# Kernel tuning notes

Measured on AMD Instinct MI355X. Metric: run time of the kernel, lower is better.

Reference implementation:

```python
import jax, jax.numpy as jnp
import numpy as np

N_DIMS = 64
D1 = N_DIMS - 1          # 63, feature dim of xs and of per-head q/k/v in non-last layers
N_EMBD = 2 * N_DIMS      # 128, forced by H + attn residual
N_LAYER = 12
N_HEAD = 4
POINTS = 512
BS = 16
LN_EPS = 1e-5


def setup_inputs() -> dict:
    key = jax.random.key(0)
    ks = jax.random.split(key, 16)
    s = 0.05
    f32 = jnp.float32
    inp = {
        "xs": jax.random.normal(ks[0], (BS, POINTS, D1), f32),
        "ys": jax.random.normal(ks[1], (BS, POINTS), f32),
        "head_mask": jnp.ones((1, N_HEAD, 1, 1), f32),
        # _read_in
        "read_in_W": jax.random.normal(ks[2], (N_DIMS, N_EMBD), f32) * s,
        "read_in_b": jnp.zeros((N_EMBD,), f32),
        # layers 0..n_layer-2: q/v Linear(D1 -> n_head*D1), key linear is unused (identity repeat)
        "qW": jax.random.normal(ks[3], (N_LAYER - 1, D1, N_HEAD * D1), f32) * s,
        "vW": jax.random.normal(ks[4], (N_LAYER - 1, D1, N_HEAD * D1), f32) * s,
        # last layer: q/k/v Linear(n_embd -> n_head*n_embd)
        "qW_last": jax.random.normal(ks[5], (N_EMBD, N_HEAD * N_EMBD), f32) * s,
        "kW_last": jax.random.normal(ks[6], (N_EMBD, N_HEAD * N_EMBD), f32) * s,
        "vW_last": jax.random.normal(ks[7], (N_EMBD, N_HEAD * N_EMBD), f32) * s,
        # layernorms
        "ln1_g": jnp.ones((N_LAYER, N_EMBD), f32),
        "ln1_b": jnp.zeros((N_LAYER, N_EMBD), f32),
        "ln2_g": jnp.ones((N_LAYER, N_EMBD), f32),
        "ln2_b": jnp.zeros((N_LAYER, N_EMBD), f32),
        # MLPs (n_embd -> 4*n_embd -> n_embd)
        "mlp_W1": jax.random.normal(ks[8], (N_LAYER, N_EMBD, 4 * N_EMBD), f32) * s,
        "mlp_b1": jnp.zeros((N_LAYER, 4 * N_EMBD), f32),
        "mlp_W2": jax.random.normal(ks[9], (N_LAYER, 4 * N_EMBD, N_EMBD), f32) * s,
        "mlp_b2": jnp.zeros((N_LAYER, N_EMBD), f32),
        # _read_out
        "read_out_W": jax.random.normal(ks[10], (N_EMBD, 1), f32) * s,
        "read_out_b": jnp.zeros((1,), f32),
    }
    return inp


def _layernorm(x, g, b):
    mu = jnp.mean(x, axis=-1, keepdims=True)
    var = jnp.var(x, axis=-1, keepdims=True)
    return (x - mu) * jax.lax.rsqrt(var + LN_EPS) * g + b


def _forward(xs, ys, head_mask, read_in_W, read_in_b, qW, vW,
             qW_last, kW_last, vW_last, ln1_g, ln1_b, ln2_g, ln2_b,
             mlp_W1, mlp_b1, mlp_W2, mlp_b2, read_out_W, read_out_b):
    bs, P, d = xs.shape  # d = n_dims - 1
    # _combine: interleave x (zero-padded) and (x, y) rows -> [bs, 2P, n_dims]
    xs_e = jnp.concatenate([xs, jnp.zeros((bs, P, 1), xs.dtype)], axis=2)
    ys_w = jnp.concatenate([xs, ys[:, :, None]], axis=2)
    zs = jnp.stack([xs_e, ys_w], axis=2).reshape(bs, 2 * P, d + 1)
    N = 2 * P

    # triangular count-normalization: row i (0-based) has 1/(i+1) on cols <= i
    i = jnp.arange(N)
    maskNorm = jnp.where(i[None, :] <= i[:, None], 1.0 / (i[:, None] + 1.0), 0.0).astype(xs.dtype)

    H = zs @ read_in_W + read_in_b  # [bs, N, n_embd]

    for idx in range(N_LAYER):
        if idx != N_LAYER - 1:
            # q from the "label half" of H, k is identity on the "feature half", v learned
            q = (H[:, :, N_DIMS:2 * N_DIMS - 1] @ qW[idx]).reshape(bs, N, N_HEAD, D1).transpose(0, 2, 1, 3)
            k = jnp.broadcast_to(H[:, None, :, :D1], (bs, N_HEAD, N, D1))
            v = (H[:, :, :D1] @ vW[idx]).reshape(bs, N, N_HEAD, D1).transpose(0, 2, 1, 3)
            # cat((z1[n_dims zeros], ., z2[1 zero])) -> head dim 2*n_dims == n_embd
            pad = ((0, 0), (0, 0), (0, 0), (N_DIMS, 1))
            q = jnp.pad(q, pad) * head_mask
            k = jnp.pad(k, pad) * head_mask
            v = jnp.pad(v, pad) * head_mask
        else:
            q = (H @ qW_last).reshape(bs, N, N_HEAD, N_EMBD).transpose(0, 2, 1, 3) * head_mask
            k = (H @ kW_last).reshape(bs, N, N_HEAD, N_EMBD).transpose(0, 2, 1, 3) * head_mask
            v = (H @ vW_last).reshape(bs, N, N_HEAD, N_EMBD).transpose(0, 2, 1, 3) * head_mask
        scores = jax.nn.relu(jnp.einsum('bhid,bhjd->bhij', q, k)) * maskNorm  # [bs,h,N,N]
        attn = jnp.einsum('bhij,bhjd->bhid', scores, v).sum(axis=1)           # [bs,N,n_embd]
        H = _layernorm(H + attn, ln1_g[idx], ln1_b[idx])
        mlp = jax.nn.relu(H @ mlp_W1[idx] + mlp_b1[idx]) @ mlp_W2[idx] + mlp_b2[idx]
        H = _layernorm(H + mlp, ln2_g[idx], ln2_b[idx])

    pred = H @ read_out_W + read_out_b  # [bs, N, 1]
    return pred[:, ::2, 0]              # [bs, P]


def reference(xs, ys, head_mask, read_in_W, read_in_b, qW, vW,
              qW_last, kW_last, vW_last, ln1_g, ln1_b, ln2_g, ln2_b,
              mlp_W1, mlp_b1, mlp_W2, mlp_b2, read_out_W, read_out_b):
    return _forward(xs, ys, head_mask, read_in_W, read_in_b, qW, vW,
                    qW_last, kW_last, vW_last, ln1_g, ln1_b, ln2_g, ln2_b,
                    mlp_W1, mlp_b1, mlp_W2, mlp_b2, read_out_W, read_out_b)
```

## Files before the change

### kernel.cpp

```cpp
#include <hip/hip_runtime.h>

#define BS 16
#define SEQ 1024
#define EMB 128
#define NHEAD 4
#define LN_EPS 1e-5f

typedef __attribute__((ext_vector_type(8))) short bf16x8;
typedef __attribute__((ext_vector_type(8))) _Float16 f16x8;
typedef __attribute__((ext_vector_type(4))) float f32x4;
typedef __attribute__((ext_vector_type(4))) unsigned short u16x4;
typedef __attribute__((ext_vector_type(4))) unsigned int u32x4;

__device__ __forceinline__ unsigned short f2b(float f) {
  union { float f; unsigned u; } v; v.f = f;
  unsigned r = v.u + 0x7fff + ((v.u >> 16) & 1);
  return (unsigned short)(r >> 16);
}
__device__ __forceinline__ float b2f(unsigned short u) {
  return __uint_as_float((unsigned)u << 16);
}
__device__ __forceinline__ unsigned short f2h(float f) {
  union { _Float16 h; unsigned short u; } v; v.h = (_Float16)f; return v.u;
}
__device__ __forceinline__ void split2(float x, unsigned short& hi, unsigned short& lo) {
  unsigned short h = f2b(x);
  float hf = __uint_as_float((unsigned)h << 16);
  hi = h; lo = f2b(x - hf);
}
__device__ __forceinline__ float rsqrt_acc(float v) {
  float r = rsqrtf(v);
  return r * (1.5f - 0.5f * v * r * r);
}

__global__ void k_prep_fragT(const float* __restrict__ in, unsigned short* __restrict__ out,
                             size_t PL, int L, int Kin, int Nin, int N, int K) {
  int idx = blockIdx.x * 256 + threadIdx.x;
  int nblk = (N >> 4) * (K >> 5);
  int total = L * N * K;
  if (idx >= total) return;
  int e = idx & 7;
  int lane = (idx >> 3) & 63;
  int blk = (idx >> 9) % nblk;
  int l = idx / (512 * nblk);
  int nb = blk % (N >> 4), kc = blk / (N >> 4);
  int n = nb * 16 + (lane & 15);
  int k = kc * 32 + (lane >> 4) * 8 + e;
  float v = (k < Kin && n < Nin) ? in[(size_t)l * Kin * Nin + (size_t)k * Nin + n] : 0.f;
  unsigned short hi, lo; split2(v, hi, lo);
  out[idx] = hi; out[PL + idx] = lo;
}

__global__ void k_prep_qvfrag(const float* __restrict__ qW, const float* __restrict__ vW,
                              unsigned short* __restrict__ out, size_t PL) {
  int idx = blockIdx.x * 256 + threadIdx.x;
  int total = 11 * 512 * 128;
  if (idx >= total) return;
  int e = idx & 7;
  int lane = (idx >> 3) & 63;
  int blk = (idx >> 9) & 127;
  int l = idx >> 16;
  int nb = blk & 31, kc = blk >> 5;
  int n = nb * 16 + (lane & 15);
  int k = kc * 32 + (lane >> 4) * 8 + e;
  float v = 0.f;
  if (n < 256) {
    int hh = n >> 6, d = n & 63;
    if (d < 63 && k >= 64 && k < 127) v = qW[(size_t)l * 63 * 252 + (size_t)(k - 64) * 252 + hh * 63 + d];
  } else {
    int n2 = n - 256, hh = n2 >> 6, d = n2 & 63;
    if (d < 63 && k < 63) v = vW[(size_t)l * 63 * 252 + (size_t)k * 252 + hh * 63 + d];
  }
  unsigned short hi, lo; split2(v, hi, lo);
  out[idx] = hi; out[PL + idx] = lo;
}

__global__ void k_prep_lastfrag(const float* __restrict__ qW, const float* __restrict__ kW,
                                const float* __restrict__ vW,
                                unsigned short* __restrict__ out, size_t PL) {
  int idx = blockIdx.x * 256 + threadIdx.x;
  int total = 1536 * 128;
  if (idx >= total) return;
  int e = idx & 7;
  int lane = (idx >> 3) & 63;
  int blk = idx >> 9;
  int nb = blk % 96, kc = blk / 96;
  int n = nb * 16 + (lane & 15);
  int k = kc * 32 + (lane >> 4) * 8 + e;
  int tsel = n >> 9, n2 = n & 511;
  const float* W = tsel == 0 ? qW : (tsel == 1 ? kW : vW);
  float v = W[(size_t)k * 512 + n2];
  unsigned short hi, lo; split2(v, hi, lo);
  out[idx] = hi; out[PL + idx] = lo;
}

__global__ void k_combine_readin(const float* __restrict__ xs, const float* __restrict__ ys,
                                 const float* __restrict__ W, const float* __restrict__ bias,
                                 unsigned short* __restrict__ Hbf, size_t hbPl,
                                 unsigned short* __restrict__ Hh) {
  int blk = blockIdx.x;
  int b = blk >> 10, t = blk & 1023, p = t >> 1;
  __shared__ float zs[64];
  int tid = threadIdx.x;
  if (tid < 64) {
    float v;
    if (tid < 63) v = xs[((size_t)b * 512 + p) * 63 + tid];
    else v = (t & 1) ? ys[(size_t)b * 512 + p] : 0.f;
    zs[tid] = v;
  }
  __syncthreads();
  float acc = bias[tid];
  #pragma unroll 8
  for (int d = 0; d < 64; ++d) acc += zs[d] * W[d * 128 + tid];
  size_t o = (size_t)blk * 128 + tid;
  unsigned short hi, lo; split2(acc, hi, lo);
  Hbf[o] = hi; Hbf[hbPl + o] = lo;
  if (tid < 64) Hh[(size_t)blk * 64 + tid] = f2h(acc);
}

template<int MODE, bool RELU>
__global__ __launch_bounds__(256) void k_gemm(
    const unsigned short* __restrict__ A, size_t aPl,
    const unsigned short* __restrict__ BT, size_t bPl, const float* __restrict__ bias,
    int N,
    unsigned short* __restrict__ out0,
    unsigned short* __restrict__ out1,
    unsigned short* __restrict__ out2) {
  extern __shared__ unsigned short lds[];
  int tid = threadIdx.x;
  int wid = tid >> 6, lane = tid & 63;
  int lr = lane & 15, lg = lane >> 4;
  int row0g = blockIdx.x * 64;
  int n0 = blockIdx.y * 64;
  unsigned short* Ah = lds;
  unsigned short* Al = Ah + 64 * 136;
  {
    const unsigned short* gA = A + (size_t)row0g * 128;
    const unsigned short* srcs[2] = { gA, gA + aPl };
    unsigned short* dsts[2] = { Ah, Al };
    #pragma unroll
    for (int p = 0; p < 2; ++p)
      #pragma unroll
      for (int it = 0; it < 4; ++it) {
        int e = it * 2048 + tid * 8;
        bf16x8 v = *reinterpret_cast<const bf16x8*>(srcs[p] + e);
        *reinterpret_cast<bf16x8*>(dsts[p] + (e >> 7) * 136 + (e & 127)) = v;
      }
  }
  __syncthreads();
  bf16x8 afh[4], afl[4];
  #pragma unroll
  for (int kf = 0; kf < 4; ++kf) {
    int o = (wid * 16 + lr) * 136 + kf * 32 + lg * 8;
    afh[kf] = *reinterpret_cast<const bf16x8*>(Ah + o);
    afl[kf] = *reinterpret_cast<const bf16x8*>(Al + o);
  }
  f32x4 acc[4] = {};
  int nhw = N >> 4;
  #pragma unroll
  for (int nf = 0; nf < 4; ++nf) {
    #pragma unroll
    for (int kf = 0; kf < 4; ++kf) {
      size_t bo = ((size_t)kf * nhw + (n0 >> 4) + nf) * 512 + lane * 8;
      bf16x8 bh = *reinterpret_cast<const bf16x8*>(BT + bo);
      bf16x8 bl = *reinterpret_cast<const bf16x8*>(BT + bPl + bo);
      acc[nf] = __builtin_amdgcn_mfma_f32_16x16x32_bf16(afh[kf], bh, acc[nf], 0, 0, 0);
      acc[nf] = __builtin_amdgcn_mfma_f32_16x16x32_bf16(afl[kf], bh, acc[nf], 0, 0, 0);
      acc[nf] = __builtin_amdgcn_mfma_f32_16x16x32_bf16(afh[kf], bl, acc[nf], 0, 0, 0);
    }
  }
  __syncthreads();
  #pragma unroll
  for (int nf = 0; nf < 4; ++nf) {
    int c = n0 + nf * 16 + lr;
    float bv = bias ? bias[c] : 0.f;
    #pragma unroll
    for (int r = 0; r < 4; ++r) {
      float v = acc[nf][r] + bv;
      if (RELU) v = fmaxf(v, 0.f);
      int rL = wid * 16 + lg * 4 + r, cL = nf * 16 + lr;
      ((unsigned short(*)[66])lds)[rL][cL] = f2h(v);
    }
  }
  __syncthreads();
  int u = tid * 2;
  int lane2 = u >> 3, e0 = u & 7;
  if (MODE == 2) {
    unsigned short (*t16)[66] = (unsigned short(*)[66])lds;
    int b = row0g >> 10, t0 = row0g & 1023;
    int tsel = n0 >> 9, c2b = n0 & 511, hh = c2b >> 7, dbase = c2b & 127;
    size_t bh = (size_t)b * NHEAD + hh;
    if (tsel < 2) {
      unsigned short* base = tsel ? out1 : out0;
      int tb0 = t0 >> 4, kc0 = dbase >> 5;
      #pragma unroll
      for (int fb = 0; fb < 8; ++fb) {
        int tbl = fb >> 1, kcl = fb & 1;
        int t_l = tbl * 16 + (lane2 & 15);
        int c_l = kcl * 32 + ((lane2 >> 4) << 3) + e0;
        size_t dst = ((bh * 64 + tb0 + tbl) * 4 + kc0 + kcl) * 512 + lane2 * 8 + e0;
        base[dst] = t16[t_l][c_l];
        base[dst + 1] = t16[t_l][c_l + 1];
      }
    } else {
      int db0 = dbase >> 4, jc0 = t0 >> 5;
      #pragma unroll
      for (int fb = 0; fb < 8; ++fb) {
        int dbl = fb >> 1, jcl = fb & 1;
        int c_l = dbl * 16 + (lane2 & 15);
        int t_l = jcl * 32 + ((lane2 >> 4) << 3) + e0;
        size_t dst = ((bh * 8 + db0 + dbl) * 32 + jc0 + jcl) * 512 + lane2 * 8 + e0;
        out2[dst] = t16[t_l][c_l];
        out2[dst + 1] = t16[t_l + 1][c_l];
      }
    }
  } else {
    unsigned short (*t16)[66] = (unsigned short(*)[66])lds;
    int b = row0g >> 10, t0 = row0g & 1023;
    if (n0 < 256) {
      size_t bh = (size_t)b * NHEAD + (n0 >> 6);
      int tb0 = t0 >> 4;
      #pragma unroll
      for (int fb = 0; fb < 8; ++fb) {
        int tbl = fb >> 1, kcl = fb & 1;
        int t_l = tbl * 16 + (lane2 & 15);
        int c_l = kcl * 32 + ((lane2 >> 4) << 3) + e0;
        size_t dst = ((bh * 64 + tb0 + tbl) * 2 + kcl) * 512 + lane2 * 8 + e0;
        out0[dst] = t16[t_l][c_l];
        out0[dst + 1] = t16[t_l][c_l + 1];
      }
    } else {
      size_t bh = (size_t)b * NHEAD + ((n0 - 256) >> 6);
      int jc0 = t0 >> 5;
      #pragma unroll
      for (int fb = 0; fb < 8; ++fb) {
        int dbl = fb >> 1, jcl = fb & 1;
        int c_l = dbl * 16 + (lane2 & 15);
        int t_l = jcl * 32 + ((lane2 >> 4) << 3) + e0;
        size_t dst = ((bh * 4 + dbl) * 32 + jc0 + jcl) * 512 + lane2 * 8 + e0;
        out1[dst] = t16[t_l][c_l];
        out1[dst + 1] = t16[t_l + 1][c_l];
      }
    }
  }
}

__global__ __launch_bounds__(512) void k_attn_v7(
    const unsigned short* __restrict__ q,
    const unsigned short* __restrict__ Hh,
    const unsigned short* __restrict__ vT,
    const float* __restrict__ head_mask,
    const unsigned short* __restrict__ HbfIn, unsigned short* __restrict__ HbfOut, size_t hbPl,
    const float* __restrict__ g, const float* __restrict__ bta) {
  extern __shared__ char sh[];
  int bid = blockIdx.x;
  int xcd = bid & 7, u = bid >> 3;
  int b = xcd * 2 + (u >> 4);
  int pidx = u & 15;
  int tid = threadIdx.x;
  int wid = tid >> 6, lane = tid & 63;
  int h = wid & 3, grp = wid >> 2;
  int lr = lane & 15, lg = lane >> 4;
  int i0t[2] = { pidx * 32, (31 - pidx) * 32 };
  int NSS = (33 - pidx) >> 1;

  const char* gK = (const char*)(Hh + (size_t)b * SEQ * 64);
  char* KB = sh;
  unsigned short* sw = (unsigned short*)(sh + 16384 + wid * 2560);

  const unsigned short* qh = q + (size_t)(b * NHEAD + h) * 65536;
  const unsigned short* vh = vT + (size_t)(b * NHEAD + h) * 65536;

  f16x8 qf[2][2][2];
  #pragma unroll
  for (int t = 0; t < 2; ++t)
    #pragma unroll
    for (int mf = 0; mf < 2; ++mf)
      #pragma unroll
      for (int kf = 0; kf < 2; ++kf)
        qf[t][mf][kf] = *reinterpret_cast<const f16x8*>(
            qh + ((((i0t[t] >> 4) + mf) * 2 + kf) << 9) + lane * 8);
  f32x4 oacc[2][2][4] = {};

  u32x4 sreg;
  auto SLOAD = [&](int ss) {
    sreg = *reinterpret_cast<const u32x4*>(gK + (size_t)ss * 8192 + tid * 16);
  };
  auto SWRITE = [&](int buf) {
    int row = tid >> 3, colb = (tid & 7) * 16;
    *reinterpret_cast<u32x4*>(KB + buf * 8192 + row * 128 + (colb ^ ((row & 7) << 4))) = sreg;
  };

  SLOAD(0); SWRITE(0);
  __syncthreads();

  for (int ss = 0; ss < NSS; ++ss) {
    int cur = ss & 1;
    bool more = (ss + 1 < NSS);
    if (more) SLOAD(ss + 1);
    int js = ss * 64 + grp * 32;
    if (js < i0t[1] + 32) {
      f16x8 vch[4];
      #pragma unroll
      for (int nf = 0; nf < 4; ++nf)
        vch[nf] = *reinterpret_cast<const f16x8*>(vh + ((nf * 32 + (js >> 5)) << 9) + lane * 8);
      f16x8 kfr[2][2];
      #pragma unroll
      for (int nf2 = 0; nf2 < 2; ++nf2)
        #pragma unroll
        for (int kf = 0; kf < 2; ++kf) {
          int row = grp * 32 + nf2 * 16 + lr;
          int colb = kf * 64 + lg * 16;
          kfr[nf2][kf] = *reinterpret_cast<const f16x8*>(
              KB + cur * 8192 + row * 128 + (colb ^ ((row & 7) << 4)));
        }
      #pragma unroll
      for (int t = 0; t < 2; ++t) {
        if (js < i0t[t] + 32) {
          #pragma unroll
          for (int nf2 = 0; nf2 < 2; ++nf2) {
            #pragma unroll
            for (int mf = 0; mf < 2; ++mf) {
              f32x4 sacc = {};
              #pragma unroll
              for (int kf = 0; kf < 2; ++kf)
                sacc = __builtin_amdgcn_mfma_f32_16x16x32_f16(qf[t][mf][kf], kfr[nf2][kf], sacc, 0, 0, 0);
              #pragma unroll
              for (int r = 0; r < 4; ++r) {
                int i = i0t[t] + mf * 16 + lg * 4 + r;
                int j = js + nf2 * 16 + lr;
                float v = (j <= i) ? fmaxf(sacc[r], 0.f) : 0.f;
                sw[(mf * 16 + lg * 4 + r) * 40 + nf2 * 16 + lr] = f2h(v);
              }
            }
          }
          asm volatile("s_waitcnt lgkmcnt(0)" ::: "memory");
          __builtin_amdgcn_sched_barrier(0);
          #pragma unroll
          for (int mf = 0; mf < 2; ++mf) {
            f16x8 sf = *reinterpret_cast<const f16x8*>(&sw[(mf * 16 + lr) * 40 + lg * 8]);
            #pragma unroll
            for (int nf = 0; nf < 4; ++nf)
              oacc[t][mf][nf] = __builtin_amdgcn_mfma_f32_16x16x32_f16(sf, vch[nf], oacc[t][mf][nf], 0, 0, 0);
          }
        }
      }
    }
    if (more) SWRITE(cur ^ 1);
    __syncthreads();
  }

  float hm = head_mask[h];
  float hm3 = hm * hm * hm;
  float* f8 = (float*)sh;
  for (int t = 0; t < 2; ++t) {
    #pragma unroll
    for (int mf = 0; mf < 2; ++mf)
      #pragma unroll
      for (int nf = 0; nf < 4; ++nf)
        #pragma unroll
        for (int r = 0; r < 4; ++r)
          f8[wid * 2048 + (mf * 16 + lg * 4 + r) * 64 + nf * 16 + lr] = oacc[t][mf][nf][r] * hm3;
    __syncthreads();
    for (int idx = tid; idx < 8192; idx += 512) f8[idx] += f8[idx + 8192];
    __syncthreads();
    for (int idx = tid; idx < 4096; idx += 512) f8[idx] += f8[idx + 4096];
    __syncthreads();
    for (int idx = tid; idx < 2048; idx += 512) {
      int rr = idx >> 6;
      f8[idx] = (f8[idx] + f8[idx + 2048]) / (float)(i0t[t] + rr + 1);
    }
    __syncthreads();
    for (int rl = 0; rl < 4; ++rl) {
      int rr = wid * 4 + rl;
      size_t row = ((size_t)b * SEQ + i0t[t] + rr) * EMB;
      int c0 = lane, c1 = lane + 64;
      float x0 = b2f(HbfIn[row + c0]) + b2f(HbfIn[hbPl + row + c0]);
      float x1 = b2f(HbfIn[row + c1]) + b2f(HbfIn[hbPl + row + c1]) + f8[rr * 64 + lane];
      float s1 = x0 + x1, s2 = x0 * x0 + x1 * x1;
      #pragma unroll
      for (int off = 1; off < 64; off <<= 1) {
        s1 += __shfl_xor(s1, off);
        s2 += __shfl_xor(s2, off);
      }
      float mu = s1 * (1.f / 128.f);
      float var = s2 * (1.f / 128.f) - mu * mu;
      float rs = rsqrt_acc(var + LN_EPS);
      float y0 = (x0 - mu) * rs * g[c0] + bta[c0];
      float y1 = (x1 - mu) * rs * g[c1] + bta[c1];
      unsigned short h0, l0, h1, l1; split2(y0, h0, l0); split2(y1, h1, l1);
      HbfOut[row + c0] = h0; HbfOut[hbPl + row + c0] = l0;
      HbfOut[row + c1] = h1; HbfOut[hbPl + row + c1] = l1;
    }
    __syncthreads();
  }
}

__global__ __launch_bounds__(512) void k_attn_fused(
    const unsigned short* __restrict__ q,
    const unsigned short* __restrict__ kbuf,
    const unsigned short* __restrict__ vT,
    const float* __restrict__ head_mask,
    const unsigned short* __restrict__ HbfIn, unsigned short* __restrict__ HbfOut, size_t hbPl,
    const float* __restrict__ g, const float* __restrict__ bta) {
  constexpr int KF = 4, NFO = 8;
  constexpr int NT = SEQ / 32;
  extern __shared__ char sh[];
  int bid = blockIdx.x;
  int xcd = bid & 7, u = bid >> 3;
  int b = xcd * 2 + (u >> 4);
  int pidx = u & 15;
  int tid = threadIdx.x;
  int wid = tid >> 6, lane = tid & 63;
  int h = wid & 3, grp = wid >> 2;
  int lr = lane & 15, lg = lane >> 4;
  unsigned short* sw = (unsigned short*)(sh + wid * 2560);
  const unsigned short* qh = q + (size_t)(b * NHEAD + h) * 131072;
  const unsigned short* kh = kbuf + (size_t)(b * NHEAD + h) * 131072;
  const unsigned short* vh = vT + (size_t)(b * NHEAD + h) * 131072;
  float hm = head_mask[h];
  float hm3 = hm * hm * hm;

  for (int s = 0; s < 2; ++s) {
    int tile = (s == 0) ? pidx : (NT - 1 - pidx);
    int i0 = tile * 32;
    f16x8 qf[2][KF];
    #pragma unroll
    for (int mf = 0; mf < 2; ++mf)
      #pragma unroll
      for (int kf = 0; kf < KF; ++kf)
        qf[mf][kf] = *reinterpret_cast<const f16x8*>(
            qh + ((((i0 >> 4) + mf) * 4 + kf) << 9) + lane * 8);
    f32x4 oacc[2][NFO] = {};
    int jend = i0 + 32;
    for (int j0 = grp * 32; j0 < jend; j0 += 64) {
      f16x8 vch[NFO];
      #pragma unroll
      for (int nf = 0; nf < NFO; ++nf)
        vch[nf] = *reinterpret_cast<const f16x8*>(vh + ((nf * 32 + (j0 >> 5)) << 9) + lane * 8);
      #pragma unroll
      for (int nf2 = 0; nf2 < 2; ++nf2) {
        f16x8 kfr[KF];
        #pragma unroll
        for (int kf = 0; kf < KF; ++kf)
          kfr[kf] = *reinterpret_cast<const f16x8*>(
              kh + ((((j0 >> 4) + nf2) * 4 + kf) << 9) + lane * 8);
        #pragma unroll
        for (int mf = 0; mf < 2; ++mf) {
          f32x4 sacc = {};
          #pragma unroll
          for (int kf = 0; kf < KF; ++kf)
            sacc = __builtin_amdgcn_mfma_f32_16x16x32_f16(qf[mf][kf], kfr[kf], sacc, 0, 0, 0);
          #pragma unroll
          for (int r = 0; r < 4; ++r) {
            int i = i0 + mf * 16 + lg * 4 + r;
            int j = j0 + nf2 * 16 + lr;
            float v = (j <= i) ? fmaxf(sacc[r], 0.f) : 0.f;
            sw[(mf * 16 + lg * 4 + r) * 40 + nf2 * 16 + lr] = f2h(v);
          }
        }
      }
      asm volatile("s_waitcnt lgkmcnt(0)" ::: "memory");
      __builtin_amdgcn_sched_barrier(0);
      #pragma unroll
      for (int mf = 0; mf < 2; ++mf) {
        f16x8 sf = *reinterpret_cast<const f16x8*>(&sw[(mf * 16 + lr) * 40 + lg * 8]);
        #pragma unroll
        for (int nf = 0; nf < NFO; ++nf)
          oacc[mf][nf] = __builtin_amdgcn_mfma_f32_16x16x32_f16(sf, vch[nf], oacc[mf][nf], 0, 0, 0);
      }
    }
    float* f8 = (float*)sh;
    __syncthreads();
    if (wid < 4) {
      #pragma unroll
      for (int mf = 0; mf < 2; ++mf)
        #pragma unroll
        for (int nf = 0; nf < NFO; ++nf)
          #pragma unroll
          for (int r = 0; r < 4; ++r)
            f8[(wid & 3) * 4096 + (mf * 16 + lg * 4 + r) * 128 + nf * 16 + lr] = oacc[mf][nf][r] * hm3;
    }
    __syncthreads();
    if (wid >= 4) {
      #pragma unroll
      for (int mf = 0; mf < 2; ++mf)
        #pragma unroll
        for (int nf = 0; nf < NFO; ++nf)
          #pragma unroll
          for (int r = 0; r < 4; ++r)
            f8[(wid & 3) * 4096 + (mf * 16 + lg * 4 + r) * 128 + nf * 16 + lr] += oacc[mf][nf][r] * hm3;
    }
    __syncthreads();
    for (int idx = tid; idx < 8192; idx += 512) f8[idx] += f8[idx + 8192];
    __syncthreads();
    for (int idx = tid; idx < 4096; idx += 512) {
      int rr = idx >> 7;
      f8[idx] = (f8[idx] + f8[idx + 4096]) / (float)(i0 + rr + 1);
    }
    __syncthreads();
    for (int rl = 0; rl < 4; ++rl) {
      int rr = wid * 4 + rl;
      size_t row = ((size_t)b * SEQ + i0 + rr) * EMB;
      int c0 = lane, c1 = lane + 64;
      float x0 = b2f(HbfIn[row + c0]) + b2f(HbfIn[hbPl + row + c0]) + f8[rr * 128 + c0];
      float x1 = b2f(HbfIn[row + c1]) + b2f(HbfIn[hbPl + row + c1]) + f8[rr * 128 + c1];
      float s1 = x0 + x1, s2 = x0 * x0 + x1 * x1;
      #pragma unroll
      for (int off = 1; off < 64; off <<= 1) {
        s1 += __shfl_xor(s1, off);
        s2 += __shfl_xor(s2, off);
      }
      float mu = s1 * (1.f / 128.f);
      float var = s2 * (1.f / 128.f) - mu * mu;
      float rs = rsqrt_acc(var + LN_EPS);
      float y0 = (x0 - mu) * rs * g[c0] + bta[c0];
      float y1 = (x1 - mu) * rs * g[c1] + bta[c1];
      unsigned short h0, l0, h1, l1; split2(y0, h0, l0); split2(y1, h1, l1);
      HbfOut[row + c0] = h0; HbfOut[hbPl + row + c0] = l0;
      HbfOut[row + c1] = h1; HbfOut[hbPl + row + c1] = l1;
    }
    __syncthreads();
  }
}

template<bool LAST>
__global__ __launch_bounds__(256) void k_mlpf(
    const unsigned short* __restrict__ A, size_t aPl,
    const unsigned short* __restrict__ W1, size_t w1Pl, const float* __restrict__ b1,
    const unsigned short* __restrict__ W2, size_t w2Pl, const float* __restrict__ b2,
    unsigned short* __restrict__ HbfOut, size_t hbPl,
    unsigned short* __restrict__ Hh, float* __restrict__ Hst,
    const float* __restrict__ g, const float* __restrict__ bta) {
  extern __shared__ unsigned short mlds[];
  unsigned short* As = mlds;
  unsigned short* Mid = mlds + 4224;
  float* yb = (float*)(mlds + 4224 + 16512);
  int tid = threadIdx.x;
  int wid = tid >> 6, lane = tid & 63;
  int lr = lane & 15, lg = lane >> 4;
  int row0g = blockIdx.x * 16;
  {
    const unsigned short* gA = A + (size_t)row0g * 128;
    int e = tid * 8;
    int ro = (e >> 7) * 132 + (e & 127);
    *reinterpret_cast<bf16x8*>(As + ro) = *reinterpret_cast<const bf16x8*>(gA + e);
    *reinterpret_cast<bf16x8*>(As + 2112 + ro) = *reinterpret_cast<const bf16x8*>(gA + aPl + e);
  }
  __syncthreads();
  bf16x8 afh[4], afl[4];
  #pragma unroll
  for (int kf = 0; kf < 4; ++kf) {
    int o = lr * 132 + kf * 32 + lg * 8;
    afh[kf] = *reinterpret_cast<const bf16x8*>(As + o);
    afl[kf] = *reinterpret_cast<const bf16x8*>(As + 2112 + o);
  }
  #pragma unroll
  for (int j = 0; j < 8; ++j) {
    int ntile = wid * 8 + j;
    f32x4 acc = {};
    #pragma unroll
    for (int kf = 0; kf < 4; ++kf) {
      size_t bo = ((size_t)kf * 32 + ntile) * 512 + lane * 8;
      bf16x8 bh = *reinterpret_cast<const bf16x8*>(W1 + bo);
      bf16x8 bl = *reinterpret_cast<const bf16x8*>(W1 + w1Pl + bo);
      acc = __builtin_amdgcn_mfma_f32_16x16x32_bf16(afh[kf], bh, acc, 0, 0, 0);
      acc = __builtin_amdgcn_mfma_f32_16x16x32_bf16(afl[kf], bh, acc, 0, 0, 0);
      acc = __builtin_amdgcn_mfma_f32_16x16x32_bf16(afh[kf], bl, acc, 0, 0, 0);
    }
    int c = ntile * 16 + lr;
    float bv = b1[c];
    #pragma unroll
    for (int r = 0; r < 4; ++r) {
      float v = fmaxf(acc[r] + bv, 0.f);
      unsigned short hi, lo; split2(v, hi, lo);
      int row = lg * 4 + r;
      Mid[row * 516 + c] = hi;
      Mid[8256 + row * 516 + c] = lo;
    }
  }
  __syncthreads();
  f32x4 acc2[2] = {};
  #pragma unroll
  for (int kc = 0; kc < 16; ++kc) {
    int o = lr * 516 + kc * 32 + lg * 8;
    bf16x8 amh = *reinterpret_cast<const bf16x8*>(Mid + o);
    bf16x8 aml = *reinterpret_cast<const bf16x8*>(Mid + 8256 + o);
    #pragma unroll
    for (int j = 0; j < 2; ++j) {
      int ntile = wid * 2 + j;
      size_t bo = ((size_t)kc * 8 + ntile) * 512 + lane * 8;
      bf16x8 bh = *reinterpret_cast<const bf16x8*>(W2 + bo);
      bf16x8 bl = *reinterpret_cast<const bf16x8*>(W2 + w2Pl + bo);
      acc2[j] = __builtin_amdgcn_mfma_f32_16x16x32_bf16(amh, bh, acc2[j], 0, 0, 0);
      acc2[j] = __builtin_amdgcn_mfma_f32_16x16x32_bf16(aml, bh, acc2[j], 0, 0, 0);
      acc2[j] = __builtin_amdgcn_mfma_f32_16x16x32_bf16(amh, bl, acc2[j], 0, 0, 0);
    }
  }
  #pragma unroll
  for (int j = 0; j < 2; ++j) {
    int c = (wid * 2 + j) * 16 + lr;
    float bv = b2[c];
    #pragma unroll
    for (int r = 0; r < 4; ++r) {
      int row = lg * 4 + r;
      float yres = b2f(As[row * 132 + c]) + b2f(As[2112 + row * 132 + c]);
      yb[row * 132 + c] = acc2[j][r] + bv + yres;
    }
  }
  __syncthreads();
  for (int rl = 0; rl < 4; ++rl) {
    int row = wid * 4 + rl;
    size_t gro = (size_t)(row0g + row) * EMB;
    int c0 = lane, c1 = lane + 64;
    float x0 = yb[row * 132 + c0];
    float x1 = yb[row * 132 + c1];
    float s1 = x0 + x1, s2 = x0 * x0 + x1 * x1;
    #pragma unroll
    for (int off = 1; off < 64; off <<= 1) {
      s1 += __shfl_xor(s1, off);
      s2 += __shfl_xor(s2, off);
    }
    float mu = s1 * (1.f / 128.f);
    float var = s2 * (1.f / 128.f) - mu * mu;
    float rs = rsqrt_acc(var + LN_EPS);
    float y0 = (x0 - mu) * rs * g[c0] + bta[c0];
    float y1 = (x1 - mu) * rs * g[c1] + bta[c1];
    unsigned short h0, l0, h1, l1; split2(y0, h0, l0); split2(y1, h1, l1);
    HbfOut[gro + c0] = h0; HbfOut[hbPl + gro + c0] = l0;
    HbfOut[gro + c1] = h1; HbfOut[hbPl + gro + c1] = l1;
    Hh[(size_t)(row0g + row) * 64 + lane] = f2h(y0);
    if (LAST) { Hst[gro + c0] = y0; Hst[gro + c1] = y1; }
  }
}

__global__ __launch_bounds__(64) void k_readout(const float* __restrict__ H,
                                                const float* __restrict__ W, const float* __restrict__ b0,
                                                float* __restrict__ out) {
  int idx = blockIdx.x;
  int b = idx >> 9, p = idx & 511;
  size_t row = ((size_t)b * SEQ + 2 * p) * EMB;
  int lane = threadIdx.x;
  float acc = H[row + lane] * W[lane] + H[row + 64 + lane] * W[64 + lane];
  #pragma unroll
  for (int off = 1; off < 64; off <<= 1) acc += __shfl_xor(acc, off);
  if (lane == 0) out[idx] = acc + b0[0];
}

extern "C" void kernel_launch(void* const* d_in, const int* in_sizes, int n_in,
                              void* d_out, int out_size, void* d_ws, size_t ws_size,
                              hipStream_t stream) {
  (void)in_sizes; (void)n_in; (void)out_size; (void)ws_size;
  const float* xs        = (const float*)d_in[0];
  const float* ys        = (const float*)d_in[1];
  const float* head_mask = (const float*)d_in[2];
  const float* read_in_W = (const float*)d_in[3];
  const float* read_in_b = (const float*)d_in[4];
  const float* qW        = (const float*)d_in[5];
  const float* vW        = (const float*)d_in[6];
  const float* qW_last   = (const float*)d_in[7];
  const float* kW_last   = (const float*)d_in[8];
  const float* vW_last   = (const float*)d_in[9];
  const float* ln1_g     = (const float*)d_in[10];
  const float* ln1_b     = (const float*)d_in[11];
  const float* ln2_g     = (const float*)d_in[12];
  const float* ln2_b     = (const float*)d_in[13];
  const float* mlp_W1    = (const float*)d_in[14];
  const float* mlp_b1    = (const float*)d_in[15];
  const float* mlp_W2    = (const float*)d_in[16];
  const float* mlp_b2    = (const float*)d_in[17];
  const float* ro_W      = (const float*)d_in[18];
  const float* ro_b      = (const float*)d_in[19];

  const size_t HPL   = (size_t)BS * SEQ * EMB;
  const size_t QVWPL = (size_t)11 * 512 * 128;
  const size_t W1PL  = (size_t)12 * 512 * 128;
  const size_t W2PL  = (size_t)12 * 512 * 128;
  const size_t LASTPL= (size_t)1536 * 128;
  const size_t VOFF  = (size_t)BS * NHEAD * 65536;

  char* ws = (char*)d_ws;
  size_t off = 0;
  auto alloc = [&](size_t bytes) -> void* {
    void* p = ws + off;
    off += (bytes + 255) & ~(size_t)255;
    return p;
  };
  float* H             = (float*)alloc(HPL * 4);
  unsigned short* Hbf  = (unsigned short*)alloc(2 * HPL * 2);
  unsigned short* Hbf2 = (unsigned short*)alloc(2 * HPL * 2);
  unsigned short* Hh   = (unsigned short*)alloc((size_t)BS * SEQ * 64 * 2);
  unsigned short* qbuf = (unsigned short*)alloc((size_t)BS * NHEAD * 131072 * 2);
  unsigned short* kmid = (unsigned short*)alloc((size_t)BS * NHEAD * 131072 * 2);
  unsigned short* vTl  = (unsigned short*)alloc((size_t)BS * NHEAD * 131072 * 2);
  unsigned short* qvWT = (unsigned short*)alloc(2 * QVWPL * 2);
  unsigned short* W1T  = (unsigned short*)alloc(2 * W1PL * 2);
  unsigned short* W2T  = (unsigned short*)alloc(2 * W2PL * 2);
  unsigned short* lastT= (unsigned short*)alloc(2 * LASTPL * 2);

  { int tot = 11 * 512 * 128; k_prep_qvfrag<<<dim3((tot + 255) / 256), 256, 0, stream>>>(qW, vW, qvWT, QVWPL); }
  { int tot = 12 * 512 * 128; k_prep_fragT<<<dim3((tot + 255) / 256), 256, 0, stream>>>(mlp_W1, W1T, W1PL, 12, 128, 512, 512, 128); }
  { int tot = 12 * 512 * 128; k_prep_fragT<<<dim3((tot + 255) / 256), 256, 0, stream>>>(mlp_W2, W2T, W2PL, 12, 512, 128, 128, 512); }
  { int tot = 1536 * 128; k_prep_lastfrag<<<dim3((tot + 255) / 256), 256, 0, stream>>>(qW_last, kW_last, vW_last, lastT, LASTPL); }

  k_combine_readin<<<dim3(BS * SEQ), 128, 0, stream>>>(xs, ys, read_in_W, read_in_b, Hbf, HPL, Hh);

  const int GEMM_LDS = 2 * 64 * 136 * 2;
  const int MLPF_LDS = (4224 + 16512) * 2 + 16 * 132 * 4;

  for (int l = 0; l < 11; ++l) {
    k_gemm<3, false><<<dim3(256, 8), 256, GEMM_LDS, stream>>>(
        Hbf, HPL, qvWT + (size_t)l * 65536, QVWPL, nullptr, 512,
        qbuf, qbuf + VOFF, nullptr);
    k_attn_v7<<<dim3(256), 512, 65536, stream>>>(
        qbuf, Hh, qbuf + VOFF, head_mask, Hbf, Hbf2, HPL, ln1_g + l * 128, ln1_b + l * 128);
    k_mlpf<false><<<dim3(1024), 256, MLPF_LDS, stream>>>(
        Hbf2, HPL, W1T + (size_t)l * 65536, W1PL, mlp_b1 + l * 512,
        W2T + (size_t)l * 65536, W2PL, mlp_b2 + l * 128,
        Hbf, HPL, Hh, nullptr, ln2_g + l * 128, ln2_b + l * 128);
  }
  k_gemm<2, false><<<dim3(256, 24), 256, GEMM_LDS, stream>>>(
      Hbf, HPL, lastT, LASTPL, nullptr, 1536, qbuf, kmid, vTl);
  k_attn_fused<<<dim3(256), 512, 65536, stream>>>(
      qbuf, kmid, vTl, head_mask, Hbf, Hbf2, HPL, ln1_g + 11 * 128, ln1_b + 11 * 128);
  k_mlpf<true><<<dim3(1024), 256, MLPF_LDS, stream>>>(
      Hbf2, HPL, W1T + (size_t)11 * 65536, W1PL, mlp_b1 + 11 * 512,
      W2T + (size_t)11 * 65536, W2PL, mlp_b2 + 11 * 128,
      Hbf, HPL, Hh, H, ln2_g + 11 * 128, ln2_b + 11 * 128);

  k_readout<<<dim3(8192), 64, 0, stream>>>(H, ro_W, ro_b, (float*)d_out);
}
```

Baseline: 1.110 ms.

## Swizzle MLP LDS layouts, prefetch weight fragments, alias output buffer

In the fused MLP kernel, the input tile's LDS layout changes from padded rows to an XOR-swizzled layout. The intermediate activations are now stored in MFMA fragment order so the second GEMM reads them with one contiguous vector load per lane. W1 and W2 fragments are software-prefetched one tile ahead into registers so global loads overlap the MFMAs. The float output staging buffer now aliases the Mid region behind an added barrier, which shrinks LDS per block to raise occupancy but adds register pressure.

```diff
diff --git a/kernel.cpp b/kernel.cpp
--- a/kernel.cpp
+++ b/kernel.cpp
@@ -534,69 +534,104 @@
     const float* __restrict__ g, const float* __restrict__ bta) {
   extern __shared__ unsigned short mlds[];
   unsigned short* As = mlds;
-  unsigned short* Mid = mlds + 4224;
-  float* yb = (float*)(mlds + 4224 + 16512);
+  unsigned short* Mid = mlds + 4096;
+  float* yb = (float*)Mid;
   int tid = threadIdx.x;
   int wid = tid >> 6, lane = tid & 63;
   int lr = lane & 15, lg = lane >> 4;
   int row0g = blockIdx.x * 16;
   {
     const unsigned short* gA = A + (size_t)row0g * 128;
-    int e = tid * 8;
-    int ro = (e >> 7) * 132 + (e & 127);
-    *reinterpret_cast<bf16x8*>(As + ro) = *reinterpret_cast<const bf16x8*>(gA + e);
-    *reinterpret_cast<bf16x8*>(As + 2112 + ro) = *reinterpret_cast<const bf16x8*>(gA + aPl + e);
+    int row = tid >> 4;
+    int sc = ((tid & 15) * 8) ^ ((row & 7) << 3);
+    *reinterpret_cast<bf16x8*>(As + row * 128 + sc) =
+        *reinterpret_cast<const bf16x8*>(gA + tid * 8);
+    *reinterpret_cast<bf16x8*>(As + 2048 + row * 128 + sc) =
+        *reinterpret_cast<const bf16x8*>(gA + aPl + tid * 8);
   }
   __syncthreads();
   bf16x8 afh[4], afl[4];
   #pragma unroll
   for (int kf = 0; kf < 4; ++kf) {
-    int o = lr * 132 + kf * 32 + lg * 8;
+    int o = lr * 128 + ((kf * 32 + lg * 8) ^ ((lr & 7) << 3));
     afh[kf] = *reinterpret_cast<const bf16x8*>(As + o);
-    afl[kf] = *reinterpret_cast<const bf16x8*>(As + 2112 + o);
+    afl[kf] = *reinterpret_cast<const bf16x8*>(As + 2048 + o);
+  }
+  bf16x8 cwh[4], cwl[4], nwh[4], nwl[4];
+  #pragma unroll
+  for (int kf = 0; kf < 4; ++kf) {
+    size_t bo = ((size_t)kf * 32 + wid * 8) * 512 + lane * 8;
+    cwh[kf] = *reinterpret_cast<const bf16x8*>(W1 + bo);
+    cwl[kf] = *reinterpret_cast<const bf16x8*>(W1 + w1Pl + bo);
   }
   #pragma unroll
   for (int j = 0; j < 8; ++j) {
     int ntile = wid * 8 + j;
+    if (j < 7) {
+      #pragma unroll
+      for (int kf = 0; kf < 4; ++kf) {
+        size_t bo = ((size_t)kf * 32 + ntile + 1) * 512 + lane * 8;
+        nwh[kf] = *reinterpret_cast<const bf16x8*>(W1 + bo);
+        nwl[kf] = *reinterpret_cast<const bf16x8*>(W1 + w1Pl + bo);
+      }
+    }
     f32x4 acc = {};
     #pragma unroll
     for (int kf = 0; kf < 4; ++kf) {
-      size_t bo = ((size_t)kf * 32 + ntile) * 512 + lane * 8;
-      bf16x8 bh = *reinterpret_cast<const bf16x8*>(W1 + bo);
-      bf16x8 bl = *reinterpret_cast<const bf16x8*>(W1 + w1Pl + bo);
-      acc = __builtin_amdgcn_mfma_f32_16x16x32_bf16(afh[kf], bh, acc, 0, 0, 0);
-      acc = __builtin_amdgcn_mfma_f32_16x16x32_bf16(afl[kf], bh, acc, 0, 0, 0);
-      acc = __builtin_amdgcn_mfma_f32_16x16x32_bf16(afh[kf], bl, acc, 0, 0, 0);
+      acc = __builtin_amdgcn_mfma_f32_16x16x32_bf16(afh[kf], cwh[kf], acc, 0, 0, 0);
+      acc = __builtin_amdgcn_mfma_f32_16x16x32_bf16(afl[kf], cwh[kf], acc, 0, 0, 0);
+      acc = __builtin_amdgcn_mfma_f32_16x16x32_bf16(afh[kf], cwl[kf], acc, 0, 0, 0);
     }
     int c = ntile * 16 + lr;
     float bv = b1[c];
+    int kc = c >> 5, sub = ((c & 31) >> 3) * 128 + (c & 7);
     #pragma unroll
     for (int r = 0; r < 4; ++r) {
       float v = fmaxf(acc[r] + bv, 0.f);
       unsigned short hi, lo; split2(v, hi, lo);
-      int row = lg * 4 + r;
-      Mid[row * 516 + c] = hi;
-      Mid[8256 + row * 516 + c] = lo;
+      int ma = kc * 512 + sub + (lg * 4 + r) * 8;
+      Mid[ma] = hi;
+      Mid[8192 + ma] = lo;
+    }
+    if (j < 7) {
+      #pragma unroll
+      for (int kf = 0; kf < 4; ++kf) { cwh[kf] = nwh[kf]; cwl[kf] = nwl[kf]; }
     }
   }
   __syncthreads();
   f32x4 acc2[2] = {};
+  bf16x8 c2h[2], c2l[2], n2h[2], n2l[2];
+  #pragma unroll
+  for (int j = 0; j < 2; ++j) {
+    size_t bo = (size_t)(wid * 2 + j) * 512 + lane * 8;
+    c2h[j] = *reinterpret_cast<const bf16x8*>(W2 + bo);
+    c2l[j] = *reinterpret_cast<const bf16x8*>(W2 + w2Pl + bo);
+  }
   #pragma unroll
   for (int kc = 0; kc < 16; ++kc) {
-    int o = lr * 516 + kc * 32 + lg * 8;
+    if (kc < 15) {
+      #pragma unroll
+      for (int j = 0; j < 2; ++j) {
+        size_t bo = ((size_t)(kc + 1) * 8 + wid * 2 + j) * 512 + lane * 8;
+        n2h[j] = *reinterpret_cast<const bf16x8*>(W2 + bo);
+        n2l[j] = *reinterpret_cast<const bf16x8*>(W2 + w2Pl + bo);
+      }
+    }
+    int o = kc * 512 + lane * 8;
     bf16x8 amh = *reinterpret_cast<const bf16x8*>(Mid + o);
-    bf16x8 aml = *reinterpret_cast<const bf16x8*>(Mid + 8256 + o);
+    bf16x8 aml = *reinterpret_cast<const bf16x8*>(Mid + 8192 + o);
     #pragma unroll
     for (int j = 0; j < 2; ++j) {
-      int ntile = wid * 2 + j;
-      size_t bo = ((size_t)kc * 8 + ntile) * 512 + lane * 8;
-      bf16x8 bh = *reinterpret_cast<const bf16x8*>(W2 + bo);
-      bf16x8 bl = *reinterpret_cast<const bf16x8*>(W2 + w2Pl + bo);
-      acc2[j] = __builtin_amdgcn_mfma_f32_16x16x32_bf16(amh, bh, acc2[j], 0, 0, 0);
-      acc2[j] = __builtin_amdgcn_mfma_f32_16x16x32_bf16(aml, bh, acc2[j], 0, 0, 0);
-      acc2[j] = __builtin_amdgcn_mfma_f32_16x16x32_bf16(amh, bl, acc2[j], 0, 0, 0);
-    }
-  }
+      acc2[j] = __builtin_amdgcn_mfma_f32_16x16x32_bf16(amh, c2h[j], acc2[j], 0, 0, 0);
+      acc2[j] = __builtin_amdgcn_mfma_f32_16x16x32_bf16(aml, c2h[j], acc2[j], 0, 0, 0);
+      acc2[j] = __builtin_amdgcn_mfma_f32_16x16x32_bf16(amh, c2l[j], acc2[j], 0, 0, 0);
+    }
+    if (kc < 15) {
+      c2h[0] = n2h[0]; c2h[1] = n2h[1];
+      c2l[0] = n2l[0]; c2l[1] = n2l[1];
+    }
+  }
+  __syncthreads();
   #pragma unroll
   for (int j = 0; j < 2; ++j) {
     int c = (wid * 2 + j) * 16 + lr;
@@ -604,7 +639,8 @@
     #pragma unroll
     for (int r = 0; r < 4; ++r) {
       int row = lg * 4 + r;
-      float yres = b2f(As[row * 132 + c]) + b2f(As[2112 + row * 132 + c]);
+      int sc = c ^ ((row & 7) << 3);
+      float yres = b2f(As[row * 128 + sc]) + b2f(As[2048 + row * 128 + sc]);
       yb[row * 132 + c] = acc2[j][r] + bv + yres;
     }
   }
@@ -706,7 +742,7 @@
   k_combine_readin<<<dim3(BS * SEQ), 128, 0, stream>>>(xs, ys, read_in_W, read_in_b, Hbf, HPL, Hh);
 
   const int GEMM_LDS = 2 * 64 * 136 * 2;
-  const int MLPF_LDS = (4224 + 16512) * 2 + 16 * 132 * 4;
+  const int MLPF_LDS = (4096 + 16384) * 2;
 
   for (int l = 0; l < 11; ++l) {
     k_gemm<3, false><<<dim3(256, 8), 256, GEMM_LDS, stream>>>(
```

After: 925.4 us. -16.6%, faster.
